# Kernel optimization log

Hardware: AMD Instinct MI355X
Metric: run time of the kernel (lower is better)

## Reference

```python
import jax, jax.numpy as jnp
import numpy as np

B, F, NUM_LAYERS, T, DEPTH, C = 256, 128, 4, 2048, 6, 100
L = 2 ** DEPTH  # num_leaves = 64

# bit pattern of the oblivious tree: bit d of leaf_idx (MSB-first),
# matching (leaf_idx // (L >> (d+1))) % 2 in the original double loop
_BITS = np.stack([(np.arange(L) // (L >> (d + 1))) % 2 for d in range(DEPTH)])  # [DEPTH, L]


def setup_inputs() -> dict:
    key = jax.random.key(0)
    k = jax.random.split(key, 5)
    x = jax.random.normal(k[0], (B, F), dtype=jnp.float32)
    sel_W = jax.random.normal(k[1], (NUM_LAYERS, T * DEPTH, F), dtype=jnp.float32) * 0.05
    sel_b = jax.random.normal(k[2], (NUM_LAYERS, T * DEPTH), dtype=jnp.float32) * 0.01
    out_W = jax.random.normal(k[3], (C, NUM_LAYERS * T * L), dtype=jnp.float32) * 0.002
    out_b = jax.random.normal(k[4], (C,), dtype=jnp.float32) * 0.01
    return {"x": x, "sel_W": sel_W, "sel_b": sel_b, "out_W": out_W, "out_b": out_b}


def reference(x, sel_W, sel_b, out_W, out_b):
    bits = jnp.asarray(_BITS, dtype=x.dtype)  # [DEPTH, L]
    layer_outputs = []
    for i in range(NUM_LAYERS):
        # feature selector linear -> [B, T, DEPTH] threshold responses
        fv = jax.nn.sigmoid(x @ sel_W[i].T + sel_b[i]).reshape(B, T, DEPTH)
        # leaf probability = prod over depth of (left or right prob per bit)
        leaf = jnp.ones((B, T, L), dtype=x.dtype)
        for d in range(DEPTH):  # fixed small structural loop (depth=6)
            p = fv[:, :, d:d + 1]                     # [B, T, 1] left prob
            bit = bits[d]                             # [L]
            leaf = leaf * (p * (1.0 - bit) + (1.0 - p) * bit)
        layer_outputs.append(leaf.reshape(B, T * L))
    combined = jnp.concatenate(layer_outputs, axis=1)  # [B, NUM_LAYERS*T*L]
    return combined @ out_W.T + out_b
```

## Files before the change

kernel.cpp:

```cpp
#include <hip/hip_runtime.h>

#define BB 256
#define FF 128
#define NL 4
#define TT 2048
#define DD 6
#define CC 100
#define LL 64
#define RTOT 49152
#define ITOT 8192
#define CPAD 112
#define KG 512
#define ITPB 16

typedef short bf16x8 __attribute__((ext_vector_type(8)));
typedef float f32x4 __attribute__((ext_vector_type(4)));

static __device__ inline unsigned short f2bf(float f) {
    unsigned u = __float_as_uint(f);
    u += 0x7fffu + ((u >> 16) & 1u);
    return (unsigned short)(u >> 16);
}
static __device__ inline float bf2f(unsigned short h) {
    return __uint_as_float(((unsigned)h) << 16);
}

__global__ __launch_bounds__(256) void fv_kernel(
    const float* __restrict__ x, const float* __restrict__ selW,
    const float* __restrict__ selb, unsigned short* __restrict__ fv)
{
    __shared__ unsigned short wt[128 * 136];
    __shared__ unsigned short xt[128 * 136];
    __shared__ float sb[128];

    const int tid = threadIdx.x;
    const int m0 = blockIdx.x * 128;
    const int n0 = blockIdx.y * 128;

    for (int pass = 0; pass < 16; ++pass) {
        int idx = pass * 256 + tid;
        int r = idx >> 5, f4 = idx & 31;
        float4 v = *((const float4*)(selW + (size_t)(m0 + r) * FF) + f4);
        ushort4 h;
        h.x = f2bf(v.x); h.y = f2bf(v.y); h.z = f2bf(v.z); h.w = f2bf(v.w);
        *(ushort4*)(wt + r * 136 + f4 * 4) = h;
        float4 vx = *((const float4*)(x + (size_t)(n0 + r) * FF) + f4);
        ushort4 hx;
        hx.x = f2bf(vx.x); hx.y = f2bf(vx.y); hx.z = f2bf(vx.z); hx.w = f2bf(vx.w);
        *(ushort4*)(xt + r * 136 + f4 * 4) = hx;
    }
    if (tid < 128) sb[tid] = selb[m0 + tid];
    __syncthreads();

    const int w = tid >> 6, lane = tid & 63;
    const int q = lane >> 4, l15 = lane & 15;
    const int mq = w & 1, nq = w >> 1;

    f32x4 zero4 = {0.f, 0.f, 0.f, 0.f};
    f32x4 acc[4][4];
    for (int i = 0; i < 4; ++i)
        for (int j = 0; j < 4; ++j) acc[i][j] = zero4;

    for (int ch = 0; ch < 4; ++ch) {
        bf16x8 a[4];
        for (int ms = 0; ms < 4; ++ms)
            a[ms] = *(const bf16x8*)(wt + (mq * 64 + ms * 16 + l15) * 136 + ch * 32 + q * 8);
        for (int ns = 0; ns < 4; ++ns) {
            bf16x8 bfr = *(const bf16x8*)(xt + (nq * 64 + ns * 16 + l15) * 136 + ch * 32 + q * 8);
            for (int ms = 0; ms < 4; ++ms)
                acc[ms][ns] = __builtin_amdgcn_mfma_f32_16x16x32_bf16(a[ms], bfr, acc[ms][ns], 0, 0, 0);
        }
    }

    for (int ms = 0; ms < 4; ++ms) {
        int rowl = mq * 64 + ms * 16 + q * 4;
        for (int ns = 0; ns < 4; ++ns) {
            int b = n0 + nq * 64 + ns * 16 + l15;
            for (int reg = 0; reg < 4; ++reg) {
                int row = m0 + rowl + reg;
                float z = acc[ms][ns][reg] + sb[rowl + reg];
                float e = __expf(-z);
                float p = 1.0f / (1.0f + e);
                int i = row / 12288;
                int rr = row - i * 12288;
                int t = rr / 6;
                int d = rr - t * 6;
                size_t it = (size_t)i * TT + t;
                fv[it * 1536 + d * 256 + b] = f2bf(p);
            }
        }
    }
}

__global__ __launch_bounds__(256) void main_gemm(
    const unsigned short* __restrict__ fv, const float* __restrict__ outW,
    float* __restrict__ part)
{
    __shared__ unsigned short leaf[256 * 72];
    __shared__ unsigned short wt[CPAD * 72];

    const int tid = threadIdx.x;
    const int kg = blockIdx.x;
    const int w = tid >> 6, lane = tid & 63;
    const int q = lane >> 4, l15 = lane & 15;

    f32x4 zero4 = {0.f, 0.f, 0.f, 0.f};
    f32x4 acc[4][7];
    for (int i = 0; i < 4; ++i)
        for (int j = 0; j < 7; ++j) acc[i][j] = zero4;

    for (int itl = 0; itl < ITPB; ++itl) {
        const int it = kg * ITPB + itl;

        const unsigned short* fvp = fv + (size_t)it * 1536 + tid;
        float p0 = bf2f(fvp[0]);
        float p1 = bf2f(fvp[256]);
        float p2 = bf2f(fvp[512]);
        float p3 = bf2f(fvp[768]);
        float p4 = bf2f(fvp[1024]);
        float p5 = bf2f(fvp[1280]);

        {
            int cc = tid >> 4, f4 = tid & 15;
            for (int pass = 0; pass < 7; ++pass) {
                int c = pass * 16 + cc;
                float4 v = make_float4(0.f, 0.f, 0.f, 0.f);
                if (c < CC)
                    v = *((const float4*)(outW + (size_t)c * 524288 + (size_t)it * 64) + f4);
                ushort4 h;
                h.x = f2bf(v.x); h.y = f2bf(v.y); h.z = f2bf(v.z); h.w = f2bf(v.w);
                *(ushort4*)(wt + c * 72 + f4 * 4) = h;
            }
        }

        {
            float q0 = 1.f - p0, q1 = 1.f - p1, q2 = 1.f - p2;
            float q3 = 1.f - p3, q4 = 1.f - p4, q5 = 1.f - p5;
            float A[4]  = {p0 * p1, p0 * q1, q0 * p1, q0 * q1};
            float B2[4] = {p2 * p3, p2 * q3, q2 * p3, q2 * q3};
            float C2[4] = {p4 * p5, p4 * q5, q4 * p5, q4 * q5};
            float BC[16];
            for (int m = 0; m < 16; ++m) BC[m] = B2[m >> 2] * C2[m & 3];
            unsigned short* row = leaf + tid * 72;
            for (int j = 0; j < 8; ++j) {
                uint4 dw;
                unsigned int* dwp = (unsigned int*)&dw;
                for (int e = 0; e < 4; ++e) {
                    int l0 = j * 8 + 2 * e;
                    float v0 = A[l0 >> 4] * BC[l0 & 15];
                    float v1 = A[(l0 + 1) >> 4] * BC[(l0 + 1) & 15];
                    dwp[e] = (unsigned)f2bf(v0) | ((unsigned)f2bf(v1) << 16);
                }
                *(uint4*)(row + j * 8) = dw;
            }
        }
        __syncthreads();

        for (int ch = 0; ch < 2; ++ch) {
            bf16x8 a[4];
            for (int ms = 0; ms < 4; ++ms)
                a[ms] = *(const bf16x8*)(leaf + (w * 64 + ms * 16 + l15) * 72 + ch * 32 + q * 8);
            for (int nt = 0; nt < 7; ++nt) {
                bf16x8 bb = *(const bf16x8*)(wt + (nt * 16 + l15) * 72 + ch * 32 + q * 8);
                for (int ms = 0; ms < 4; ++ms)
                    acc[ms][nt] = __builtin_amdgcn_mfma_f32_16x16x32_bf16(a[ms], bb, acc[ms][nt], 0, 0, 0);
            }
        }
        __syncthreads();
    }

    float* pbase = part + (size_t)kg * (256 * CPAD);
    for (int ms = 0; ms < 4; ++ms) {
        int brow = w * 64 + ms * 16 + q * 4;
        for (int nt = 0; nt < 7; ++nt) {
            int c = nt * 16 + l15;
            for (int reg = 0; reg < 4; ++reg)
                pbase[(size_t)(brow + reg) * CPAD + c] = acc[ms][nt][reg];
        }
    }
}

__global__ __launch_bounds__(256) void reduce_k(
    const float* __restrict__ part, const float* __restrict__ outb,
    float* __restrict__ out)
{
    __shared__ float red[256];
    const int o = blockIdx.x * 64 + (threadIdx.x & 63);
    const int kq = threadIdx.x >> 6;
    const int b = o / 100, c = o - b * 100;
    const float* p = part + (size_t)b * CPAD + c + (size_t)kq * 128 * (256 * CPAD);
    float s = 0.f;
    for (int i = 0; i < 128; ++i) s += p[(size_t)i * (256 * CPAD)];
    red[threadIdx.x] = s;
    __syncthreads();
    if (threadIdx.x < 64) {
        float r = red[threadIdx.x] + red[threadIdx.x + 64] +
                  red[threadIdx.x + 128] + red[threadIdx.x + 192];
        out[o] = r + outb[c];
    }
}

extern "C" void kernel_launch(void* const* d_in, const int* in_sizes, int n_in,
                              void* d_out, int out_size, void* d_ws, size_t ws_size,
                              hipStream_t stream) {
    const float* x    = (const float*)d_in[0];
    const float* selW = (const float*)d_in[1];
    const float* selb = (const float*)d_in[2];
    const float* outW = (const float*)d_in[3];
    const float* outb = (const float*)d_in[4];
    float* out = (float*)d_out;

    unsigned short* fv = (unsigned short*)d_ws;
    float* part = (float*)((char*)d_ws + 25165824);

    fv_kernel<<<dim3(RTOT / 128, BB / 128), 256, 0, stream>>>(x, selW, selb, fv);
    main_gemm<<<KG, 256, 0, stream>>>(fv, outW, part);
    reduce_k<<<400, 256, 0, stream>>>(part, outb, out);
}
```

Measured before the change: 394.9 us.

## Prefetch next iteration's weights and probabilities into registers, restructure partial reduction layout

The main GEMM loop now loads the next iteration's out_W slice and fv probabilities into registers while the current leaf and weight tiles are being built, so global-load latency overlaps with compute. It also swaps __syncthreads for an explicit lgkmcnt-wait barrier and sets launch bounds to two blocks per CU. The partial-sum buffer is re-laid out so that each batch row's partials are contiguous, letting the reduce kernel read them with coalesced vector loads, one block per row. The fv index math is simplified to a plain row*256+b, which is equivalent to the old layout. The register prefetch raises register pressure, and the final iteration issues a redundant wrapped-around load.

```diff
diff --git a/kernel.cpp b/kernel.cpp
--- a/kernel.cpp
+++ b/kernel.cpp
@@ -2,19 +2,14 @@
 
 #define BB 256
 #define FF 128
-#define NL 4
-#define TT 2048
-#define DD 6
 #define CC 100
-#define LL 64
-#define RTOT 49152
-#define ITOT 8192
-#define CPAD 112
 #define KG 512
 #define ITPB 16
 
 typedef short bf16x8 __attribute__((ext_vector_type(8)));
 typedef float f32x4 __attribute__((ext_vector_type(4)));
+
+#define LDS_BARRIER() asm volatile("s_waitcnt lgkmcnt(0)\n\ts_barrier" ::: "memory")
 
 static __device__ inline unsigned short f2bf(float f) {
     unsigned u = __float_as_uint(f);
@@ -27,7 +22,7 @@
 
 __global__ __launch_bounds__(256) void fv_kernel(
     const float* __restrict__ x, const float* __restrict__ selW,
-    const float* __restrict__ selb, unsigned short* __restrict__ fv)
+    const float* __restrict__ selb, unsigned short* __restrict__ fvout)
 {
     __shared__ unsigned short wt[128 * 136];
     __shared__ unsigned short xt[128 * 136];
@@ -37,6 +32,7 @@
     const int m0 = blockIdx.x * 128;
     const int n0 = blockIdx.y * 128;
 
+    #pragma unroll 4
     for (int pass = 0; pass < 16; ++pass) {
         int idx = pass * 256 + tid;
         int r = idx >> 5, f4 = idx & 31;
@@ -58,93 +54,109 @@
 
     f32x4 zero4 = {0.f, 0.f, 0.f, 0.f};
     f32x4 acc[4][4];
+    #pragma unroll
     for (int i = 0; i < 4; ++i)
+        #pragma unroll
         for (int j = 0; j < 4; ++j) acc[i][j] = zero4;
 
+    #pragma unroll
     for (int ch = 0; ch < 4; ++ch) {
         bf16x8 a[4];
+        #pragma unroll
         for (int ms = 0; ms < 4; ++ms)
             a[ms] = *(const bf16x8*)(wt + (mq * 64 + ms * 16 + l15) * 136 + ch * 32 + q * 8);
+        #pragma unroll
         for (int ns = 0; ns < 4; ++ns) {
             bf16x8 bfr = *(const bf16x8*)(xt + (nq * 64 + ns * 16 + l15) * 136 + ch * 32 + q * 8);
+            #pragma unroll
             for (int ms = 0; ms < 4; ++ms)
                 acc[ms][ns] = __builtin_amdgcn_mfma_f32_16x16x32_bf16(a[ms], bfr, acc[ms][ns], 0, 0, 0);
         }
     }
 
+    #pragma unroll
     for (int ms = 0; ms < 4; ++ms) {
         int rowl = mq * 64 + ms * 16 + q * 4;
+        #pragma unroll
         for (int ns = 0; ns < 4; ++ns) {
             int b = n0 + nq * 64 + ns * 16 + l15;
+            #pragma unroll
             for (int reg = 0; reg < 4; ++reg) {
                 int row = m0 + rowl + reg;
                 float z = acc[ms][ns][reg] + sb[rowl + reg];
-                float e = __expf(-z);
-                float p = 1.0f / (1.0f + e);
-                int i = row / 12288;
-                int rr = row - i * 12288;
-                int t = rr / 6;
-                int d = rr - t * 6;
-                size_t it = (size_t)i * TT + t;
-                fv[it * 1536 + d * 256 + b] = f2bf(p);
-            }
-        }
-    }
-}
-
-__global__ __launch_bounds__(256) void main_gemm(
+                float p = 1.0f / (1.0f + __expf(-z));
+                fvout[(size_t)row * 256 + b] = f2bf(p);
+            }
+        }
+    }
+}
+
+__global__ __launch_bounds__(256, 2) void main_gemm(
     const unsigned short* __restrict__ fv, const float* __restrict__ outW,
     float* __restrict__ part)
 {
     __shared__ unsigned short leaf[256 * 72];
-    __shared__ unsigned short wt[CPAD * 72];
+    __shared__ unsigned short wt[112 * 72];
 
     const int tid = threadIdx.x;
     const int kg = blockIdx.x;
     const int w = tid >> 6, lane = tid & 63;
     const int q = lane >> 4, l15 = lane & 15;
+    const int cc = tid >> 4, f4 = tid & 15;
 
     f32x4 zero4 = {0.f, 0.f, 0.f, 0.f};
     f32x4 acc[4][7];
+    #pragma unroll
     for (int i = 0; i < 4; ++i)
+        #pragma unroll
         for (int j = 0; j < 7; ++j) acc[i][j] = zero4;
 
+    float4 wv[7];
+    unsigned short pv[6];
+    {
+        const int it = kg * ITPB;
+        #pragma unroll
+        for (int pass = 0; pass < 7; ++pass) {
+            const int c = pass * 16 + cc;
+            float4 v = make_float4(0.f, 0.f, 0.f, 0.f);
+            if (c < CC)
+                v = *((const float4*)(outW + (size_t)c * 524288 + (size_t)it * 64) + f4);
+            wv[pass] = v;
+        }
+        const unsigned short* fp = fv + (size_t)it * 1536 + tid;
+        #pragma unroll
+        for (int d = 0; d < 6; ++d) pv[d] = fp[d * 256];
+    }
+
     for (int itl = 0; itl < ITPB; ++itl) {
-        const int it = kg * ITPB + itl;
-
-        const unsigned short* fvp = fv + (size_t)it * 1536 + tid;
-        float p0 = bf2f(fvp[0]);
-        float p1 = bf2f(fvp[256]);
-        float p2 = bf2f(fvp[512]);
-        float p3 = bf2f(fvp[768]);
-        float p4 = bf2f(fvp[1024]);
-        float p5 = bf2f(fvp[1280]);
+        LDS_BARRIER();
+
+        #pragma unroll
+        for (int pass = 0; pass < 7; ++pass) {
+            const int c = pass * 16 + cc;
+            ushort4 h;
+            h.x = f2bf(wv[pass].x); h.y = f2bf(wv[pass].y);
+            h.z = f2bf(wv[pass].z); h.w = f2bf(wv[pass].w);
+            *(ushort4*)(wt + c * 72 + f4 * 4) = h;
+        }
 
         {
-            int cc = tid >> 4, f4 = tid & 15;
-            for (int pass = 0; pass < 7; ++pass) {
-                int c = pass * 16 + cc;
-                float4 v = make_float4(0.f, 0.f, 0.f, 0.f);
-                if (c < CC)
-                    v = *((const float4*)(outW + (size_t)c * 524288 + (size_t)it * 64) + f4);
-                ushort4 h;
-                h.x = f2bf(v.x); h.y = f2bf(v.y); h.z = f2bf(v.z); h.w = f2bf(v.w);
-                *(ushort4*)(wt + c * 72 + f4 * 4) = h;
-            }
-        }
-
-        {
+            float p0 = bf2f(pv[0]), p1 = bf2f(pv[1]), p2 = bf2f(pv[2]);
+            float p3 = bf2f(pv[3]), p4 = bf2f(pv[4]), p5 = bf2f(pv[5]);
             float q0 = 1.f - p0, q1 = 1.f - p1, q2 = 1.f - p2;
             float q3 = 1.f - p3, q4 = 1.f - p4, q5 = 1.f - p5;
             float A[4]  = {p0 * p1, p0 * q1, q0 * p1, q0 * q1};
             float B2[4] = {p2 * p3, p2 * q3, q2 * p3, q2 * q3};
             float C2[4] = {p4 * p5, p4 * q5, q4 * p5, q4 * q5};
             float BC[16];
+            #pragma unroll
             for (int m = 0; m < 16; ++m) BC[m] = B2[m >> 2] * C2[m & 3];
             unsigned short* row = leaf + tid * 72;
+            #pragma unroll
             for (int j = 0; j < 8; ++j) {
                 uint4 dw;
                 unsigned int* dwp = (unsigned int*)&dw;
+                #pragma unroll
                 for (int e = 0; e < 4; ++e) {
                     int l0 = j * 8 + 2 * e;
                     float v0 = A[l0 >> 4] * BC[l0 & 15];
@@ -154,28 +166,47 @@
                 *(uint4*)(row + j * 8) = dw;
             }
         }
-        __syncthreads();
-
+
+        {
+            const int itn = kg * ITPB + ((itl + 1) & (ITPB - 1));
+            #pragma unroll
+            for (int pass = 0; pass < 7; ++pass) {
+                const int c = pass * 16 + cc;
+                if (c < CC)
+                    wv[pass] = *((const float4*)(outW + (size_t)c * 524288 + (size_t)itn * 64) + f4);
+            }
+            const unsigned short* fp = fv + (size_t)itn * 1536 + tid;
+            #pragma unroll
+            for (int d = 0; d < 6; ++d) pv[d] = fp[d * 256];
+        }
+
+        LDS_BARRIER();
+
+        #pragma unroll
         for (int ch = 0; ch < 2; ++ch) {
             bf16x8 a[4];
+            #pragma unroll
             for (int ms = 0; ms < 4; ++ms)
                 a[ms] = *(const bf16x8*)(leaf + (w * 64 + ms * 16 + l15) * 72 + ch * 32 + q * 8);
+            #pragma unroll
             for (int nt = 0; nt < 7; ++nt) {
                 bf16x8 bb = *(const bf16x8*)(wt + (nt * 16 + l15) * 72 + ch * 32 + q * 8);
+                #pragma unroll
                 for (int ms = 0; ms < 4; ++ms)
                     acc[ms][nt] = __builtin_amdgcn_mfma_f32_16x16x32_bf16(a[ms], bb, acc[ms][nt], 0, 0, 0);
             }
         }
-        __syncthreads();
-    }
-
-    float* pbase = part + (size_t)kg * (256 * CPAD);
+    }
+
+    #pragma unroll
     for (int ms = 0; ms < 4; ++ms) {
-        int brow = w * 64 + ms * 16 + q * 4;
+        const int brow = w * 64 + ms * 16 + q * 4;
+        #pragma unroll
         for (int nt = 0; nt < 7; ++nt) {
-            int c = nt * 16 + l15;
+            const int c = nt * 16 + l15;
+            #pragma unroll
             for (int reg = 0; reg < 4; ++reg)
-                pbase[(size_t)(brow + reg) * CPAD + c] = acc[ms][nt][reg];
+                part[((size_t)(brow + reg) * KG + kg) * 112 + c] = acc[ms][nt][reg];
         }
     }
 }
@@ -184,19 +215,32 @@
     const float* __restrict__ part, const float* __restrict__ outb,
     float* __restrict__ out)
 {
-    __shared__ float red[256];
-    const int o = blockIdx.x * 64 + (threadIdx.x & 63);
-    const int kq = threadIdx.x >> 6;
-    const int b = o / 100, c = o - b * 100;
-    const float* p = part + (size_t)b * CPAD + c + (size_t)kq * 128 * (256 * CPAD);
-    float s = 0.f;
-    for (int i = 0; i < 128; ++i) s += p[(size_t)i * (256 * CPAD)];
-    red[threadIdx.x] = s;
+    __shared__ float red[9 * 112];
+    const int b = blockIdx.x;
+    const int tid = threadIdx.x;
+    const float* slice = part + (size_t)b * (KG * 112);
+
+    if (tid < 252) {
+        const int kgsub = tid / 28;
+        const int c4 = tid - kgsub * 28;
+        f32x4 s = {0.f, 0.f, 0.f, 0.f};
+        #pragma unroll 8
+        for (int i = 0; i < 56; ++i) {
+            f32x4 v = *((const f32x4*)slice + (i * 252 + tid));
+            s += v;
+        }
+        if (kgsub < 8) {
+            f32x4 v = *((const f32x4*)slice + ((504 + kgsub) * 28 + c4));
+            s += v;
+        }
+        *(f32x4*)(red + kgsub * 112 + c4 * 4) = s;
+    }
     __syncthreads();
-    if (threadIdx.x < 64) {
-        float r = red[threadIdx.x] + red[threadIdx.x + 64] +
-                  red[threadIdx.x + 128] + red[threadIdx.x + 192];
-        out[o] = r + outb[c];
+    if (tid < CC) {
+        float r = outb[tid];
+        #pragma unroll
+        for (int k = 0; k < 9; ++k) r += red[k * 112 + tid];
+        out[b * CC + tid] = r;
     }
 }
 
@@ -213,7 +257,7 @@
     unsigned short* fv = (unsigned short*)d_ws;
     float* part = (float*)((char*)d_ws + 25165824);
 
-    fv_kernel<<<dim3(RTOT / 128, BB / 128), 256, 0, stream>>>(x, selW, selb, fv);
+    fv_kernel<<<dim3(384, 2), 256, 0, stream>>>(x, selW, selb, fv);
     main_gemm<<<KG, 256, 0, stream>>>(fv, outW, part);
-    reduce_k<<<400, 256, 0, stream>>>(part, outb, out);
-}
+    reduce_k<<<BB, 256, 0, stream>>>(part, outb, out);
+}
```

Measured after the change: 355.5 us. 10.0% less time.
